# Kernel optimization log

Hardware: AMD Instinct MI355X
Metric: run time of the kernel (lower is better)

## Reference

```python
import jax, jax.numpy as jnp
import numpy as np

N, E, F, D, H, HID, OUT, G = 25000, 400000, 128, 16, 64, 128, 32, 64

def silu(v):
    return v * jax.nn.sigmoid(v)

def setup_inputs() -> dict:
    key = jax.random.key(0)
    ks = jax.random.split(key, 32)
    inp = {
        'x': jax.random.normal(ks[0], (N, F), jnp.float32),
        'pos': jax.random.normal(ks[1], (N, 3), jnp.float32),
        'edge_attr': jax.random.normal(ks[2], (E, D), jnp.float32),
        'edge_index': jax.random.randint(ks[3], (2, E), 0, N, jnp.int64),
        'batch': jnp.sort(jax.random.randint(ks[4], (N,), 0, G, jnp.int64)),
    }
    def lin(k, fan_in, fan_out):
        return jax.random.normal(k, (fan_in, fan_out), jnp.float32) / np.sqrt(fan_in)
    i = 5
    for l, in_c in enumerate([F, HID]):
        cat = 2 * in_c + D + 1
        inp[f'l{l}_mlp_w'] = lin(ks[i], cat, H); i += 1
        inp[f'l{l}_edge_w'] = lin(ks[i], H, H); i += 1
        inp[f'l{l}_edge_b'] = jnp.zeros((H,), jnp.float32)
        inp[f'l{l}_coord_w'] = lin(ks[i], H, 1); i += 1
        inp[f'l{l}_coord_b'] = jnp.zeros((1,), jnp.float32)
        inp[f'l{l}_node_w1'] = lin(ks[i], in_c + H, H); i += 1
        inp[f'l{l}_node_b1'] = jnp.zeros((H,), jnp.float32)
        inp[f'l{l}_node_w2'] = lin(ks[i], H, HID); i += 1
        inp[f'l{l}_node_b2'] = jnp.zeros((HID,), jnp.float32)
    inp['out_w1'] = lin(ks[i], HID, HID); i += 1
    inp['out_b1'] = jnp.zeros((HID,), jnp.float32)
    inp['out_w2'] = lin(ks[i], HID, OUT); i += 1
    inp['out_b2'] = jnp.zeros((OUT,), jnp.float32)
    return inp

def egnn_layer(x, pos, src, dst, edge_attr, mlp_w, edge_w, edge_b, coord_w, coord_b, nw1, nb1, nw2, nb2):
    # PyG flow source_to_target: i = dst (edge_index[1]), j = src (edge_index[0])
    diff = pos[dst] - pos[src]                    # (E,3)
    radial = jnp.sum(diff * diff, axis=1, keepdims=True)  # (E,1)
    cat = jnp.concatenate([x[dst], x[src], edge_attr, radial], axis=1)
    h = silu(cat @ mlp_w)                         # (E,H)
    e_ij = silu(h @ edge_w + edge_b)              # (E,H)
    coord_update = diff * silu(e_ij @ coord_w + coord_b)  # (E,3)
    e_agg = jax.ops.segment_sum(e_ij, dst, num_segments=N)          # sum reduce
    cu_sum = jax.ops.segment_sum(coord_update, dst, num_segments=N)
    deg = jax.ops.segment_sum(jnp.ones((E, 1), x.dtype), dst, num_segments=N)
    cu_mean = cu_sum / jnp.maximum(deg, 1.0)      # mean reduce, 0 for isolated nodes
    h_node = silu(jnp.concatenate([x, e_agg], axis=1) @ nw1 + nb1) @ nw2 + nb2
    return h_node, pos + cu_mean

def reference(x, pos, edge_attr, edge_index, batch,
              l0_mlp_w, l0_edge_w, l0_edge_b, l0_coord_w, l0_coord_b, l0_node_w1, l0_node_b1, l0_node_w2, l0_node_b2,
              l1_mlp_w, l1_edge_w, l1_edge_b, l1_coord_w, l1_coord_b, l1_node_w1, l1_node_b1, l1_node_w2, l1_node_b2,
              out_w1, out_b1, out_w2, out_b2):
    src, dst = edge_index[0], edge_index[1]
    x, pos = egnn_layer(x, pos, src, dst, edge_attr, l0_mlp_w, l0_edge_w, l0_edge_b, l0_coord_w, l0_coord_b, l0_node_w1, l0_node_b1, l0_node_w2, l0_node_b2)
    x, pos = egnn_layer(x, pos, src, dst, edge_attr, l1_mlp_w, l1_edge_w, l1_edge_b, l1_coord_w, l1_coord_b, l1_node_w1, l1_node_b1, l1_node_w2, l1_node_b2)
    # graph mean pooling over batch assignment
    g_sum = jax.ops.segment_sum(x, batch, num_segments=G)
    g_cnt = jax.ops.segment_sum(jnp.ones((N, 1), x.dtype), batch, num_segments=G)
    g = g_sum / jnp.maximum(g_cnt, 1.0)           # (G, HID)
    g = jax.nn.relu(g)
    return jax.nn.relu(g @ out_w1 + out_b1) @ out_w2 + out_b2  # (G, OUT)
```

## Files before the change

kernel.cpp:

```cpp
#include <hip/hip_runtime.h>
#include <math.h>

#define NN 25000
#define EE 400000
#define FF 128
#define DD 16
#define HH 64
#define HIDC 128
#define OUTC 32
#define GG 64
#define NODEBLK 782
#define SCATBLK 1563

typedef __attribute__((ext_vector_type(8))) short short8;
typedef __attribute__((ext_vector_type(8))) unsigned short u16x8;
typedef __attribute__((ext_vector_type(4))) float f32x4;

union S8 { short8 v; unsigned short u[8]; };
union U8 { u16x8 v; unsigned short u[8]; };

__device__ __forceinline__ float silu_f(float v) {
    return v / (1.f + __expf(-v));
}

__device__ __forceinline__ unsigned short f2bf_rne(float f) {
  unsigned u = __float_as_uint(f);
  unsigned r = u + 0x7fffu + ((u >> 16) & 1u);
  return (unsigned short)(r >> 16);
}
__device__ __forceinline__ float bfbits2f(unsigned short b) {
  return __uint_as_float(((unsigned)b) << 16);
}

__global__ __launch_bounds__(256) void k_hist(
    const int* __restrict__ ei, int* __restrict__ cnt) {
  const int t = blockIdx.x * 256 + threadIdx.x;
  if (t < EE) atomicAdd(&cnt[ei[EE + t]], 1);
}

__global__ __launch_bounds__(1024) void k_scan(
    const int* __restrict__ cnt, int* __restrict__ row_ptr, int* __restrict__ next) {
  __shared__ int s[1024];
  const int t = threadIdx.x;
  const int base = t * 25;
  int loc[25];
  int sum = 0;
#pragma unroll
  for (int i = 0; i < 25; ++i) {
    const int n = base + i;
    loc[i] = (n < NN) ? cnt[n] : 0;
    sum += loc[i];
  }
  s[t] = sum;
  __syncthreads();
  for (int off = 1; off < 1024; off <<= 1) {
    const int v = (t >= off) ? s[t - off] : 0;
    __syncthreads();
    s[t] += v;
    __syncthreads();
  }
  int run = s[t] - sum;
#pragma unroll
  for (int i = 0; i < 25; ++i) {
    const int n = base + i;
    if (n < NN) {
      row_ptr[n] = run;
      next[n] = run;
      run += loc[i];
    }
  }
  if (t == 0) row_ptr[NN] = EE;
}

__global__ __launch_bounds__(256) void k_sp(
    const int* __restrict__ ei, int* __restrict__ next,
    int* __restrict__ sdst, int* __restrict__ ssrc, int* __restrict__ seid,
    const float* __restrict__ X, const float* __restrict__ W,
    float* __restrict__ P1, unsigned short* __restrict__ P2h) {
  __shared__ __align__(16) float xT[4][128 * 12];
  if (blockIdx.x >= NODEBLK) {
    const int t = (blockIdx.x - NODEBLK) * 256 + threadIdx.x;
    if (t < EE) {
      const int d = ei[EE + t];
      const int slot = atomicAdd(&next[d], 1);
      sdst[slot] = d;
      ssrc[slot] = ei[t];
      seid[slot] = t;
    }
    return;
  }
  const int w = threadIdx.x >> 6, lane = threadIdx.x & 63;
  float* xt = xT[w];
  const int nb = (blockIdx.x * 4 + w) * 8;
#pragma unroll
  for (int e = 0; e < 8; ++e) {
    const int n = nb + e;
    const bool v = n < NN;
    xt[lane * 12 + e]        = v ? X[n * FF + lane] : 0.f;
    xt[(lane + 64) * 12 + e] = v ? X[n * FF + 64 + lane] : 0.f;
  }
  __syncthreads();
  float a1[8], a2[8];
#pragma unroll
  for (int e = 0; e < 8; ++e) { a1[e] = 0.f; a2[e] = 0.f; }
#pragma unroll 4
  for (int k = 0; k < 128; ++k) {
    const float wa = W[k * 64 + lane];
    const float wb = W[(128 + k) * 64 + lane];
    float xk[8];
    *(f32x4*)&xk[0] = *(const f32x4*)&xt[k * 12];
    *(f32x4*)&xk[4] = *(const f32x4*)&xt[k * 12 + 4];
#pragma unroll
    for (int e = 0; e < 8; ++e) {
      a1[e] = fmaf(xk[e], wa, a1[e]);
      a2[e] = fmaf(xk[e], wb, a2[e]);
    }
  }
#pragma unroll
  for (int e = 0; e < 8; ++e) {
    const int n = nb + e;
    if (n < NN) {
      P1[n * 64 + lane]  = a1[e];
      P2h[n * 64 + lane] = f2bf_rne(a2[e]);
    }
  }
}

template <bool COORD, bool GATHER>
__global__ __launch_bounds__(256, 4) void k_edge(
    const float* __restrict__ P1, const unsigned short* __restrict__ P2h,
    const float* __restrict__ pos, const float* __restrict__ eattr,
    float* __restrict__ seattr, const int* __restrict__ seid,
    const int* __restrict__ sdst, const int* __restrict__ ssrc,
    const float* __restrict__ mlp_w,
    const float* __restrict__ edge_w, const float* __restrict__ edge_b,
    const float* __restrict__ coord_w, const float* __restrict__ coord_b,
    float* __restrict__ e_agg, float* __restrict__ cu) {
  __shared__ __align__(16) float s_hs[4][16 * 76];
  __shared__ float s_diff[4][48];
  __shared__ float s_rad[4][16];
  __shared__ float s_red[4][16];
  const int tid = threadIdx.x, w = tid >> 6, lane = tid & 63;
  const int q = lane >> 4, m = lane & 15;

  S8 wB[2][4];
#pragma unroll
  for (int kc = 0; kc < 2; ++kc)
#pragma unroll
    for (int nc = 0; nc < 4; ++nc)
#pragma unroll
      for (int j = 0; j < 8; ++j)
        wB[kc][nc].u[j] = f2bf_rne(edge_w[(kc * 32 + q * 8 + j) * 64 + nc * 16 + m]);
  S8 w3B[4];
#pragma unroll
  for (int nc = 0; nc < 4; ++nc)
#pragma unroll
    for (int j = 0; j < 8; ++j)
      w3B[nc].u[j] = (lane < 32) ? f2bf_rne(mlp_w[256 * 64 + (q * 8 + j) * 64 + nc * 16 + m])
                                 : (unsigned short)0;
  float w4r[4], cwr[4], ebr[4];
#pragma unroll
  for (int nc = 0; nc < 4; ++nc) {
    w4r[nc] = mlp_w[272 * 64 + nc * 16 + m];
    ebr[nc] = edge_b[nc * 16 + m];
    cwr[nc] = COORD ? coord_w[nc * 16 + m] : 0.f;
  }
  const float cb = COORD ? coord_b[0] : 0.f;

  const int wave_id = blockIdx.x * 4 + w;
  const int g0 = wave_id * 6 + (wave_id < 424 ? wave_id : 424);
  const int ng = (wave_id < 424) ? 7 : 6;

  const int pe = (lane < 48) ? (lane / 3) : 0;
  const int pc = lane - (lane / 3) * 3;

  int cur_dst = -1;
  float accum = 0.f;

  for (int g = 0; g < ng; ++g) {
    const int eb = (g0 + g) * 16;
    const int dm = sdst[eb + m];
    const int sm = ssrc[eb + m];
    f32x4 p1a[2], p1b[2];
    U8 p2r[2];
#pragma unroll
    for (int kc = 0; kc < 2; ++kc) {
      const float* pp1 = P1 + (size_t)dm * 64 + kc * 32 + q * 8;
      p1a[kc] = *(const f32x4*)pp1;
      p1b[kc] = *(const f32x4*)(pp1 + 4);
      p2r[kc].v = *(const u16x8*)(P2h + (size_t)sm * 64 + kc * 32 + q * 8);
    }
    if (lane < 48) {
      const int de = __shfl(dm, pe, 64), se = __shfl(sm, pe, 64);
      s_diff[w][lane] = pos[de * 3 + pc] - pos[se * 3 + pc];
    }
    f32x4 ea0 = {0.f, 0.f, 0.f, 0.f}, ea1 = {0.f, 0.f, 0.f, 0.f};
    if (lane < 32) {
      if (GATHER) {
        const int eid = seid[eb + m];
        const float* ep = &eattr[(size_t)eid * DD + q * 8];
        ea0 = *(const f32x4*)ep;
        ea1 = *(const f32x4*)(ep + 4);
        float* sp = &seattr[(size_t)(eb + m) * DD + q * 8];
        *(f32x4*)sp = ea0;
        *(f32x4*)(sp + 4) = ea1;
      } else {
        const float* ep = &seattr[(size_t)(eb + m) * DD + q * 8];
        ea0 = *(const f32x4*)ep;
        ea1 = *(const f32x4*)(ep + 4);
      }
    }
    S8 eaA;
#pragma unroll
    for (int j = 0; j < 4; ++j) {
      eaA.u[j]     = f2bf_rne(ea0[j]);
      eaA.u[4 + j] = f2bf_rne(ea1[j]);
    }
    if (lane < 16) {
      const float d0 = s_diff[w][lane * 3 + 0];
      const float d1 = s_diff[w][lane * 3 + 1];
      const float d2 = s_diff[w][lane * 3 + 2];
      s_rad[w][lane] = fmaf(d0, d0, fmaf(d1, d1, d2 * d2));
    }
    float radr[4];
#pragma unroll
    for (int r = 0; r < 4; ++r) radr[r] = s_rad[w][q * 4 + r];
    f32x4 c3[4];
#pragma unroll
    for (int nc = 0; nc < 4; ++nc) {
      f32x4 z = {0.f, 0.f, 0.f, 0.f};
      c3[nc] = __builtin_amdgcn_mfma_f32_16x16x32_bf16(eaA.v, w3B[nc].v, z, 0, 0, 0);
    }
#pragma unroll
    for (int nc = 0; nc < 4; ++nc)
#pragma unroll
      for (int r = 0; r < 4; ++r)
        s_hs[w][(q * 4 + r) * 76 + nc * 16 + m] = fmaf(radr[r], w4r[nc], c3[nc][r]);
    S8 ahi[2], alo[2];
#pragma unroll
    for (int kc = 0; kc < 2; ++kc) {
      const float* hp = &s_hs[w][m * 76 + kc * 32 + q * 8];
      f32x4 h0 = *(const f32x4*)hp;
      f32x4 h1 = *(const f32x4*)(hp + 4);
      h0 = h0 + p1a[kc];
      h1 = h1 + p1b[kc];
      float hv[8];
      *(f32x4*)&hv[0] = h0;
      *(f32x4*)&hv[4] = h1;
#pragma unroll
      for (int j = 0; j < 8; ++j) {
        const float h = silu_f(hv[j] + bfbits2f(p2r[kc].u[j]));
        const unsigned short hb = (unsigned short)(__float_as_uint(h) >> 16);
        ahi[kc].u[j] = hb;
        alo[kc].u[j] = f2bf_rne(h - bfbits2f(hb));
      }
    }
    f32x4 o[4];
#pragma unroll
    for (int nc = 0; nc < 4; ++nc) {
      f32x4 bi = {ebr[nc], ebr[nc], ebr[nc], ebr[nc]};
      o[nc] = bi;
    }
#pragma unroll
    for (int kc = 0; kc < 2; ++kc)
#pragma unroll
      for (int nc = 0; nc < 4; ++nc) {
        o[nc] = __builtin_amdgcn_mfma_f32_16x16x32_bf16(ahi[kc].v, wB[kc][nc].v, o[nc], 0, 0, 0);
        o[nc] = __builtin_amdgcn_mfma_f32_16x16x32_bf16(alo[kc].v, wB[kc][nc].v, o[nc], 0, 0, 0);
      }
#pragma unroll
    for (int nc = 0; nc < 4; ++nc)
#pragma unroll
      for (int r = 0; r < 4; ++r) o[nc][r] = silu_f(o[nc][r]);
    if (COORD) {
#pragma unroll
      for (int r = 0; r < 4; ++r) {
        float v = o[0][r] * cwr[0] + o[1][r] * cwr[1] + o[2][r] * cwr[2] + o[3][r] * cwr[3];
        v += __shfl_xor(v, 1, 64);
        v += __shfl_xor(v, 2, 64);
        v += __shfl_xor(v, 4, 64);
        v += __shfl_xor(v, 8, 64);
        if (m == 0) s_red[w][q * 4 + r] = v;
      }
    }
#pragma unroll
    for (int nc = 0; nc < 4; ++nc)
#pragma unroll
      for (int r = 0; r < 4; ++r)
        s_hs[w][(q * 4 + r) * 76 + nc * 16 + m] = o[nc][r];
    for (int e = 0; e < 16; ++e) {
      const int dv = __shfl(dm, e, 64);
      const float v = s_hs[w][e * 76 + lane];
      if (dv == cur_dst) {
        accum += v;
      } else {
        if (cur_dst >= 0) atomicAdd(&e_agg[(size_t)cur_dst * 64 + lane], accum);
        cur_dst = dv;
        accum = v;
      }
    }
    if (COORD) {
      if (lane < 48) {
        const float s = silu_f(s_red[w][pe] + cb);
        atomicAdd(&cu[(size_t)__shfl(dm, pe, 64) * 3 + pc], s_diff[w][lane] * s);
      }
    }
  }
  if (cur_dst >= 0) atomicAdd(&e_agg[(size_t)cur_dst * 64 + lane], accum);
}

__global__ __launch_bounds__(256) void k_node_l0(
    const float* __restrict__ x_in, float* __restrict__ e_agg,
    const float* __restrict__ nw1, const float* __restrict__ nb1,
    const float* __restrict__ nw2, const float* __restrict__ nb2,
    const float* __restrict__ pos_in, const float* __restrict__ cu,
    const int* __restrict__ row_ptr,
    float* __restrict__ x_out, float* __restrict__ pos_out,
    const float* __restrict__ Wn, float* __restrict__ P1,
    unsigned short* __restrict__ P2h) {
  __shared__ __align__(16) float xT[4][192 * 12];
  const int w = threadIdx.x >> 6, lane = threadIdx.x & 63;
  float* xt = xT[w];
  const int nb = (blockIdx.x * 4 + w) * 8;
#pragma unroll
  for (int e = 0; e < 8; ++e) {
    const int n = nb + e;
    const bool v = n < NN;
    xt[lane * 12 + e]         = v ? x_in[n * HIDC + lane] : 0.f;
    xt[(64 + lane) * 12 + e]  = v ? x_in[n * HIDC + 64 + lane] : 0.f;
    xt[(128 + lane) * 12 + e] = v ? e_agg[n * 64 + lane] : 0.f;
    if (v) e_agg[n * 64 + lane] = 0.f;
  }
  __syncthreads();
  float a[8];
#pragma unroll
  for (int e = 0; e < 8; ++e) a[e] = nb1[lane];
#pragma unroll 2
  for (int k = 0; k < 192; ++k) {
    const float wv = nw1[k * 64 + lane];
    float xk[8];
    *(f32x4*)&xk[0] = *(const f32x4*)&xt[k * 12];
    *(f32x4*)&xk[4] = *(const f32x4*)&xt[k * 12 + 4];
#pragma unroll
    for (int e = 0; e < 8; ++e) a[e] = fmaf(xk[e], wv, a[e]);
  }
#pragma unroll
  for (int e = 0; e < 8; ++e) a[e] = silu_f(a[e]);
  {
    f32x4 t0 = {a[0], a[1], a[2], a[3]};
    f32x4 t1 = {a[4], a[5], a[6], a[7]};
    *(f32x4*)&xt[lane * 12]     = t0;
    *(f32x4*)&xt[lane * 12 + 4] = t1;
  }
  float olo[8], ohi[8];
#pragma unroll
  for (int e = 0; e < 8; ++e) { olo[e] = nb2[lane]; ohi[e] = nb2[64 + lane]; }
#pragma unroll 2
  for (int k = 0; k < 64; ++k) {
    const float wl = nw2[k * HIDC + lane];
    const float wh = nw2[k * HIDC + 64 + lane];
    float hk[8];
    *(f32x4*)&hk[0] = *(const f32x4*)&xt[k * 12];
    *(f32x4*)&hk[4] = *(const f32x4*)&xt[k * 12 + 4];
#pragma unroll
    for (int e = 0; e < 8; ++e) {
      olo[e] = fmaf(hk[e], wl, olo[e]);
      ohi[e] = fmaf(hk[e], wh, ohi[e]);
    }
  }
#pragma unroll
  for (int e = 0; e < 8; ++e) {
    const int n = nb + e;
    if (n < NN) {
      x_out[n * HIDC + lane]      = olo[e];
      x_out[n * HIDC + 64 + lane] = ohi[e];
    }
  }
#pragma unroll
  for (int e = 0; e < 8; ++e) {
    const int n = nb + e;
    if (n < NN && lane < 3) {
      const float dg = fmaxf((float)(row_ptr[n + 1] - row_ptr[n]), 1.f);
      pos_out[n * 3 + lane] = pos_in[n * 3 + lane] + cu[n * 3 + lane] / dg;
    }
  }
  {
    f32x4 t0 = {olo[0], olo[1], olo[2], olo[3]};
    f32x4 t1 = {olo[4], olo[5], olo[6], olo[7]};
    *(f32x4*)&xt[lane * 12]     = t0;
    *(f32x4*)&xt[lane * 12 + 4] = t1;
    f32x4 t2 = {ohi[0], ohi[1], ohi[2], ohi[3]};
    f32x4 t3 = {ohi[4], ohi[5], ohi[6], ohi[7]};
    *(f32x4*)&xt[(64 + lane) * 12]     = t2;
    *(f32x4*)&xt[(64 + lane) * 12 + 4] = t3;
  }
  float a1[8], a2[8];
#pragma unroll
  for (int e = 0; e < 8; ++e) { a1[e] = 0.f; a2[e] = 0.f; }
#pragma unroll 4
  for (int k = 0; k < 128; ++k) {
    const float wa = Wn[k * 64 + lane];
    const float wb2 = Wn[(128 + k) * 64 + lane];
    float xk[8];
    *(f32x4*)&xk[0] = *(const f32x4*)&xt[k * 12];
    *(f32x4*)&xk[4] = *(const f32x4*)&xt[k * 12 + 4];
#pragma unroll
    for (int e = 0; e < 8; ++e) {
      a1[e] = fmaf(xk[e], wa, a1[e]);
      a2[e] = fmaf(xk[e], wb2, a2[e]);
    }
  }
#pragma unroll
  for (int e = 0; e < 8; ++e) {
    const int n = nb + e;
    if (n < NN) {
      P1[n * 64 + lane]  = a1[e];
      P2h[n * 64 + lane] = f2bf_rne(a2[e]);
    }
  }
}

__global__ __launch_bounds__(256) void k_node_l1(
    const float* __restrict__ x_in, const float* __restrict__ e_agg,
    const float* __restrict__ nw1, const float* __restrict__ nb1,
    const float* __restrict__ nw2, const float* __restrict__ nb2,
    const int* __restrict__ batch,
    float* __restrict__ g_sum, float* __restrict__ g_cnt) {
  __shared__ __align__(16) float xT[4][192 * 12];
  const int w = threadIdx.x >> 6, lane = threadIdx.x & 63;
  float* xt = xT[w];
  const int nb = (blockIdx.x * 4 + w) * 8;
#pragma unroll
  for (int e = 0; e < 8; ++e) {
    const int n = nb + e;
    const bool v = n < NN;
    xt[lane * 12 + e]         = v ? x_in[n * HIDC + lane] : 0.f;
    xt[(64 + lane) * 12 + e]  = v ? x_in[n * HIDC + 64 + lane] : 0.f;
    xt[(128 + lane) * 12 + e] = v ? e_agg[n * 64 + lane] : 0.f;
  }
  __syncthreads();
  float a[8];
#pragma unroll
  for (int e = 0; e < 8; ++e) a[e] = nb1[lane];
#pragma unroll 2
  for (int k = 0; k < 192; ++k) {
    const float wv = nw1[k * 64 + lane];
    float xk[8];
    *(f32x4*)&xk[0] = *(const f32x4*)&xt[k * 12];
    *(f32x4*)&xk[4] = *(const f32x4*)&xt[k * 12 + 4];
#pragma unroll
    for (int e = 0; e < 8; ++e) a[e] = fmaf(xk[e], wv, a[e]);
  }
#pragma unroll
  for (int e = 0; e < 8; ++e) a[e] = silu_f(a[e]);
  {
    f32x4 t0 = {a[0], a[1], a[2], a[3]};
    f32x4 t1 = {a[4], a[5], a[6], a[7]};
    *(f32x4*)&xt[lane * 12]     = t0;
    *(f32x4*)&xt[lane * 12 + 4] = t1;
  }
  float olo[8], ohi[8];
#pragma unroll
  for (int e = 0; e < 8; ++e) { olo[e] = nb2[lane]; ohi[e] = nb2[64 + lane]; }
#pragma unroll 2
  for (int k = 0; k < 64; ++k) {
    const float wl = nw2[k * HIDC + lane];
    const float wh = nw2[k * HIDC + 64 + lane];
    float hk[8];
    *(f32x4*)&hk[0] = *(const f32x4*)&xt[k * 12];
    *(f32x4*)&hk[4] = *(const f32x4*)&xt[k * 12 + 4];
#pragma unroll
    for (int e = 0; e < 8; ++e) {
      olo[e] = fmaf(hk[e], wl, olo[e]);
      ohi[e] = fmaf(hk[e], wh, ohi[e]);
    }
  }
  int curb = -1;
  float accL = 0.f, accH = 0.f, c = 0.f;
#pragma unroll
  for (int e = 0; e < 8; ++e) {
    const int n = nb + e;
    if (n < NN) {
      const int bg = batch[n];
      if (bg != curb) {
        if (curb >= 0) {
          atomicAdd(&g_sum[curb * HIDC + lane], accL);
          atomicAdd(&g_sum[curb * HIDC + 64 + lane], accH);
          if (lane == 0) atomicAdd(&g_cnt[curb], c);
        }
        curb = bg; accL = olo[e]; accH = ohi[e]; c = 1.f;
      } else {
        accL += olo[e]; accH += ohi[e]; c += 1.f;
      }
    }
  }
  if (curb >= 0) {
    atomicAdd(&g_sum[curb * HIDC + lane], accL);
    atomicAdd(&g_sum[curb * HIDC + 64 + lane], accH);
    if (lane == 0) atomicAdd(&g_cnt[curb], c);
  }
}

__global__ __launch_bounds__(128) void k_final(
    const float* __restrict__ g_sum, const float* __restrict__ g_cnt,
    const float* __restrict__ w1, const float* __restrict__ b1,
    const float* __restrict__ w2, const float* __restrict__ b2,
    float* __restrict__ out) {
  __shared__ float sg[128];
  __shared__ float sh[128];
  const int g = blockIdx.x, j = threadIdx.x;
  const float c = fmaxf(g_cnt[g], 1.f);
  sg[j] = fmaxf(g_sum[g * HIDC + j] / c, 0.f);
  __syncthreads();
  float a = b1[j];
  for (int k = 0; k < 128; ++k) a += sg[k] * w1[k * 128 + j];
  sh[j] = fmaxf(a, 0.f);
  __syncthreads();
  if (j < OUTC) {
    float o = b2[j];
    for (int k = 0; k < 128; ++k) o += sh[k] * w2[k * OUTC + j];
    out[g * OUTC + j] = o;
  }
}

extern "C" void kernel_launch(void* const* d_in, const int* in_sizes, int n_in,
                              void* d_out, int out_size, void* d_ws, size_t ws_size,
                              hipStream_t stream) {
  const float* x     = (const float*)d_in[0];
  const float* pos   = (const float*)d_in[1];
  const float* eattr = (const float*)d_in[2];
  const int*   ei    = (const int*)d_in[3];
  const int*   batch = (const int*)d_in[4];
  const float* mlp_w[2]   = {(const float*)d_in[5],  (const float*)d_in[14]};
  const float* edge_w[2]  = {(const float*)d_in[6],  (const float*)d_in[15]};
  const float* edge_b[2]  = {(const float*)d_in[7],  (const float*)d_in[16]};
  const float* coord_w[2] = {(const float*)d_in[8],  (const float*)d_in[17]};
  const float* coord_b[2] = {(const float*)d_in[9],  (const float*)d_in[18]};
  const float* nw1[2]     = {(const float*)d_in[10], (const float*)d_in[19]};
  const float* nb1[2]     = {(const float*)d_in[11], (const float*)d_in[20]};
  const float* nw2[2]     = {(const float*)d_in[12], (const float*)d_in[21]};
  const float* nb2[2]     = {(const float*)d_in[13], (const float*)d_in[22]};
  const float* ow1 = (const float*)d_in[23];
  const float* ob1 = (const float*)d_in[24];
  const float* ow2 = (const float*)d_in[25];
  const float* ob2 = (const float*)d_in[26];
  float* out = (float*)d_out;

  char* p = (char*)d_ws;
  auto alloc = [&](size_t bytes) {
    void* r = (void*)p;
    p += (bytes + 255) & ~(size_t)255;
    return r;
  };
  float* P1            = (float*)alloc((size_t)NN * 64 * 4);
  unsigned short* P2h  = (unsigned short*)alloc((size_t)NN * 64 * 2);
  char* zero_base      = p;
  float* e_agg         = (float*)alloc((size_t)NN * 64 * 4);
  float* cu            = (float*)alloc((size_t)NN * 3 * 4);
  float* g_sum         = (float*)alloc((size_t)GG * HIDC * 4);
  float* g_cnt         = (float*)alloc((size_t)GG * 4);
  int* cnt             = (int*)alloc((size_t)NN * 4);
  const size_t zero_sz = (size_t)(p - zero_base);
  int* row_ptr         = (int*)alloc((size_t)(NN + 1) * 4);
  int* nxt             = (int*)alloc((size_t)NN * 4);
  int* sdst            = (int*)alloc((size_t)EE * 4);
  int* ssrc            = (int*)alloc((size_t)EE * 4);
  int* seid            = (int*)alloc((size_t)EE * 4);
  float* seattr        = (float*)alloc((size_t)EE * DD * 4);
  float* x1            = (float*)alloc((size_t)NN * HIDC * 4);
  float* pos1          = (float*)alloc((size_t)NN * 3 * 4);

  const int edgeBlocks = 1024;

  (void)hipMemsetAsync(zero_base, 0, zero_sz, stream);

  k_hist<<<SCATBLK, 256, 0, stream>>>(ei, cnt);
  k_scan<<<1, 1024, 0, stream>>>(cnt, row_ptr, nxt);
  k_sp<<<NODEBLK + SCATBLK, 256, 0, stream>>>(ei, nxt, sdst, ssrc, seid,
      x, mlp_w[0], P1, P2h);

  k_edge<true, true><<<edgeBlocks, 256, 0, stream>>>(P1, P2h, pos, eattr,
      seattr, seid, sdst, ssrc, mlp_w[0], edge_w[0], edge_b[0],
      coord_w[0], coord_b[0], e_agg, cu);
  k_node_l0<<<NODEBLK, 256, 0, stream>>>(x, e_agg, nw1[0], nb1[0],
      nw2[0], nb2[0], pos, cu, row_ptr, x1, pos1, mlp_w[1], P1, P2h);

  k_edge<false, false><<<edgeBlocks, 256, 0, stream>>>(P1, P2h, pos1, eattr,
      seattr, seid, sdst, ssrc, mlp_w[1], edge_w[1], edge_b[1],
      coord_w[1], coord_b[1], e_agg, cu);
  k_node_l1<<<NODEBLK, 256, 0, stream>>>(x1, e_agg, nw1[1], nb1[1],
      nw2[1], nb2[1], batch, g_sum, g_cnt);

  k_final<<<GG, 128, 0, stream>>>(g_sum, g_cnt, ow1, ob1, ow2, ob2, out);
}
```

Baseline: 507.9 us.

## Move node MLPs to split-bf16 MFMA and store edge attributes as bf16

```diff
diff --git a/kernel.cpp b/kernel.cpp
--- a/kernel.cpp
+++ b/kernel.cpp
@@ -11,6 +11,7 @@
 #define GG 64
 #define NODEBLK 782
 #define SCATBLK 1563
+#define NTILES 1563
 
 typedef __attribute__((ext_vector_type(8))) short short8;
 typedef __attribute__((ext_vector_type(8))) unsigned short u16x8;
@@ -30,6 +31,35 @@
 }
 __device__ __forceinline__ float bfbits2f(unsigned short b) {
   return __uint_as_float(((unsigned)b) << 16);
+}
+
+__device__ __forceinline__ void split8(const float* hv, S8& hi, S8& lo) {
+#pragma unroll
+  for (int j = 0; j < 8; ++j) {
+    const unsigned short hb = (unsigned short)(__float_as_uint(hv[j]) >> 16);
+    hi.u[j] = hb;
+    lo.u[j] = f2bf_rne(hv[j] - bfbits2f(hb));
+  }
+}
+
+__device__ __forceinline__ void loadBsplit(const float* __restrict__ W, int ldw,
+                                           int k0, int n0, int q, int m,
+                                           S8& bh, S8& bl) {
+#pragma unroll
+  for (int j = 0; j < 8; ++j) {
+    const float wv = W[(size_t)(k0 + q * 8 + j) * ldw + n0 + m];
+    const unsigned short hb = (unsigned short)(__float_as_uint(wv) >> 16);
+    bh.u[j] = hb;
+    bl.u[j] = f2bf_rne(wv - bfbits2f(hb));
+  }
+}
+
+__device__ __forceinline__ f32x4 mfma3(const S8& ah, const S8& al,
+                                       const S8& bh, const S8& bl, f32x4 c) {
+  c = __builtin_amdgcn_mfma_f32_16x16x32_bf16(ah.v, bh.v, c, 0, 0, 0);
+  c = __builtin_amdgcn_mfma_f32_16x16x32_bf16(al.v, bh.v, c, 0, 0, 0);
+  c = __builtin_amdgcn_mfma_f32_16x16x32_bf16(ah.v, bl.v, c, 0, 0, 0);
+  return c;
 }
 
 __global__ __launch_bounds__(256) void k_hist(
@@ -130,7 +160,7 @@
 __global__ __launch_bounds__(256, 4) void k_edge(
     const float* __restrict__ P1, const unsigned short* __restrict__ P2h,
     const float* __restrict__ pos, const float* __restrict__ eattr,
-    float* __restrict__ seattr, const int* __restrict__ seid,
+    unsigned short* __restrict__ seattr_h, const int* __restrict__ seid,
     const int* __restrict__ sdst, const int* __restrict__ ssrc,
     const float* __restrict__ mlp_w,
     const float* __restrict__ edge_w, const float* __restrict__ edge_b,
@@ -194,27 +224,24 @@
       const int de = __shfl(dm, pe, 64), se = __shfl(sm, pe, 64);
       s_diff[w][lane] = pos[de * 3 + pc] - pos[se * 3 + pc];
     }
-    f32x4 ea0 = {0.f, 0.f, 0.f, 0.f}, ea1 = {0.f, 0.f, 0.f, 0.f};
+    S8 eaA;
+#pragma unroll
+    for (int j = 0; j < 8; ++j) eaA.u[j] = 0;
     if (lane < 32) {
       if (GATHER) {
         const int eid = seid[eb + m];
         const float* ep = &eattr[(size_t)eid * DD + q * 8];
-        ea0 = *(const f32x4*)ep;
-        ea1 = *(const f32x4*)(ep + 4);
-        float* sp = &seattr[(size_t)(eb + m) * DD + q * 8];
-        *(f32x4*)sp = ea0;
-        *(f32x4*)(sp + 4) = ea1;
+        const f32x4 ea0 = *(const f32x4*)ep;
+        const f32x4 ea1 = *(const f32x4*)(ep + 4);
+#pragma unroll
+        for (int j = 0; j < 4; ++j) {
+          eaA.u[j]     = f2bf_rne(ea0[j]);
+          eaA.u[4 + j] = f2bf_rne(ea1[j]);
+        }
+        *(short8*)&seattr_h[(size_t)(eb + m) * DD + q * 8] = eaA.v;
       } else {
-        const float* ep = &seattr[(size_t)(eb + m) * DD + q * 8];
-        ea0 = *(const f32x4*)ep;
-        ea1 = *(const f32x4*)(ep + 4);
-      }
-    }
-    S8 eaA;
-#pragma unroll
-    for (int j = 0; j < 4; ++j) {
-      eaA.u[j]     = f2bf_rne(ea0[j]);
-      eaA.u[4 + j] = f2bf_rne(ea1[j]);
+        eaA.v = *(const short8*)&seattr_h[(size_t)(eb + m) * DD + q * 8];
+      }
     }
     if (lane < 16) {
       const float d0 = s_diff[w][lane * 3 + 0];
@@ -309,7 +336,8 @@
   if (cur_dst >= 0) atomicAdd(&e_agg[(size_t)cur_dst * 64 + lane], accum);
 }
 
-__global__ __launch_bounds__(256) void k_node_l0(
+template <bool L0>
+__global__ __launch_bounds__(256) void k_node(
     const float* __restrict__ x_in, float* __restrict__ e_agg,
     const float* __restrict__ nw1, const float* __restrict__ nb1,
     const float* __restrict__ nw2, const float* __restrict__ nb2,
@@ -317,187 +345,152 @@
     const int* __restrict__ row_ptr,
     float* __restrict__ x_out, float* __restrict__ pos_out,
     const float* __restrict__ Wn, float* __restrict__ P1,
-    unsigned short* __restrict__ P2h) {
-  __shared__ __align__(16) float xT[4][192 * 12];
-  const int w = threadIdx.x >> 6, lane = threadIdx.x & 63;
-  float* xt = xT[w];
-  const int nb = (blockIdx.x * 4 + w) * 8;
-#pragma unroll
-  for (int e = 0; e < 8; ++e) {
-    const int n = nb + e;
-    const bool v = n < NN;
-    xt[lane * 12 + e]         = v ? x_in[n * HIDC + lane] : 0.f;
-    xt[(64 + lane) * 12 + e]  = v ? x_in[n * HIDC + 64 + lane] : 0.f;
-    xt[(128 + lane) * 12 + e] = v ? e_agg[n * 64 + lane] : 0.f;
-    if (v) e_agg[n * 64 + lane] = 0.f;
-  }
-  __syncthreads();
-  float a[8];
-#pragma unroll
-  for (int e = 0; e < 8; ++e) a[e] = nb1[lane];
-#pragma unroll 2
-  for (int k = 0; k < 192; ++k) {
-    const float wv = nw1[k * 64 + lane];
-    float xk[8];
-    *(f32x4*)&xk[0] = *(const f32x4*)&xt[k * 12];
-    *(f32x4*)&xk[4] = *(const f32x4*)&xt[k * 12 + 4];
-#pragma unroll
-    for (int e = 0; e < 8; ++e) a[e] = fmaf(xk[e], wv, a[e]);
-  }
-#pragma unroll
-  for (int e = 0; e < 8; ++e) a[e] = silu_f(a[e]);
-  {
-    f32x4 t0 = {a[0], a[1], a[2], a[3]};
-    f32x4 t1 = {a[4], a[5], a[6], a[7]};
-    *(f32x4*)&xt[lane * 12]     = t0;
-    *(f32x4*)&xt[lane * 12 + 4] = t1;
-  }
-  float olo[8], ohi[8];
-#pragma unroll
-  for (int e = 0; e < 8; ++e) { olo[e] = nb2[lane]; ohi[e] = nb2[64 + lane]; }
-#pragma unroll 2
-  for (int k = 0; k < 64; ++k) {
-    const float wl = nw2[k * HIDC + lane];
-    const float wh = nw2[k * HIDC + 64 + lane];
-    float hk[8];
-    *(f32x4*)&hk[0] = *(const f32x4*)&xt[k * 12];
-    *(f32x4*)&hk[4] = *(const f32x4*)&xt[k * 12 + 4];
-#pragma unroll
-    for (int e = 0; e < 8; ++e) {
-      olo[e] = fmaf(hk[e], wl, olo[e]);
-      ohi[e] = fmaf(hk[e], wh, ohi[e]);
-    }
-  }
-#pragma unroll
-  for (int e = 0; e < 8; ++e) {
-    const int n = nb + e;
-    if (n < NN) {
-      x_out[n * HIDC + lane]      = olo[e];
-      x_out[n * HIDC + 64 + lane] = ohi[e];
-    }
-  }
-#pragma unroll
-  for (int e = 0; e < 8; ++e) {
-    const int n = nb + e;
-    if (n < NN && lane < 3) {
-      const float dg = fmaxf((float)(row_ptr[n + 1] - row_ptr[n]), 1.f);
-      pos_out[n * 3 + lane] = pos_in[n * 3 + lane] + cu[n * 3 + lane] / dg;
-    }
-  }
-  {
-    f32x4 t0 = {olo[0], olo[1], olo[2], olo[3]};
-    f32x4 t1 = {olo[4], olo[5], olo[6], olo[7]};
-    *(f32x4*)&xt[lane * 12]     = t0;
-    *(f32x4*)&xt[lane * 12 + 4] = t1;
-    f32x4 t2 = {ohi[0], ohi[1], ohi[2], ohi[3]};
-    f32x4 t3 = {ohi[4], ohi[5], ohi[6], ohi[7]};
-    *(f32x4*)&xt[(64 + lane) * 12]     = t2;
-    *(f32x4*)&xt[(64 + lane) * 12 + 4] = t3;
-  }
-  float a1[8], a2[8];
-#pragma unroll
-  for (int e = 0; e < 8; ++e) { a1[e] = 0.f; a2[e] = 0.f; }
-#pragma unroll 4
-  for (int k = 0; k < 128; ++k) {
-    const float wa = Wn[k * 64 + lane];
-    const float wb2 = Wn[(128 + k) * 64 + lane];
-    float xk[8];
-    *(f32x4*)&xk[0] = *(const f32x4*)&xt[k * 12];
-    *(f32x4*)&xk[4] = *(const f32x4*)&xt[k * 12 + 4];
-#pragma unroll
-    for (int e = 0; e < 8; ++e) {
-      a1[e] = fmaf(xk[e], wa, a1[e]);
-      a2[e] = fmaf(xk[e], wb2, a2[e]);
-    }
-  }
-#pragma unroll
-  for (int e = 0; e < 8; ++e) {
-    const int n = nb + e;
-    if (n < NN) {
-      P1[n * 64 + lane]  = a1[e];
-      P2h[n * 64 + lane] = f2bf_rne(a2[e]);
-    }
-  }
-}
-
-__global__ __launch_bounds__(256) void k_node_l1(
-    const float* __restrict__ x_in, const float* __restrict__ e_agg,
-    const float* __restrict__ nw1, const float* __restrict__ nb1,
-    const float* __restrict__ nw2, const float* __restrict__ nb2,
+    unsigned short* __restrict__ P2h,
     const int* __restrict__ batch,
     float* __restrict__ g_sum, float* __restrict__ g_cnt) {
-  __shared__ __align__(16) float xT[4][192 * 12];
-  const int w = threadIdx.x >> 6, lane = threadIdx.x & 63;
-  float* xt = xT[w];
-  const int nb = (blockIdx.x * 4 + w) * 8;
-#pragma unroll
-  for (int e = 0; e < 8; ++e) {
-    const int n = nb + e;
-    const bool v = n < NN;
-    xt[lane * 12 + e]         = v ? x_in[n * HIDC + lane] : 0.f;
-    xt[(64 + lane) * 12 + e]  = v ? x_in[n * HIDC + 64 + lane] : 0.f;
-    xt[(128 + lane) * 12 + e] = v ? e_agg[n * 64 + lane] : 0.f;
-  }
-  __syncthreads();
-  float a[8];
-#pragma unroll
-  for (int e = 0; e < 8; ++e) a[e] = nb1[lane];
-#pragma unroll 2
-  for (int k = 0; k < 192; ++k) {
-    const float wv = nw1[k * 64 + lane];
-    float xk[8];
-    *(f32x4*)&xk[0] = *(const f32x4*)&xt[k * 12];
-    *(f32x4*)&xk[4] = *(const f32x4*)&xt[k * 12 + 4];
-#pragma unroll
-    for (int e = 0; e < 8; ++e) a[e] = fmaf(xk[e], wv, a[e]);
-  }
-#pragma unroll
-  for (int e = 0; e < 8; ++e) a[e] = silu_f(a[e]);
-  {
-    f32x4 t0 = {a[0], a[1], a[2], a[3]};
-    f32x4 t1 = {a[4], a[5], a[6], a[7]};
-    *(f32x4*)&xt[lane * 12]     = t0;
-    *(f32x4*)&xt[lane * 12 + 4] = t1;
-  }
-  float olo[8], ohi[8];
-#pragma unroll
-  for (int e = 0; e < 8; ++e) { olo[e] = nb2[lane]; ohi[e] = nb2[64 + lane]; }
-#pragma unroll 2
-  for (int k = 0; k < 64; ++k) {
-    const float wl = nw2[k * HIDC + lane];
-    const float wh = nw2[k * HIDC + 64 + lane];
-    float hk[8];
-    *(f32x4*)&hk[0] = *(const f32x4*)&xt[k * 12];
-    *(f32x4*)&hk[4] = *(const f32x4*)&xt[k * 12 + 4];
-#pragma unroll
-    for (int e = 0; e < 8; ++e) {
-      olo[e] = fmaf(hk[e], wl, olo[e]);
-      ohi[e] = fmaf(hk[e], wh, ohi[e]);
-    }
-  }
-  int curb = -1;
-  float accL = 0.f, accH = 0.f, c = 0.f;
-#pragma unroll
-  for (int e = 0; e < 8; ++e) {
-    const int n = nb + e;
-    if (n < NN) {
-      const int bg = batch[n];
-      if (bg != curb) {
-        if (curb >= 0) {
-          atomicAdd(&g_sum[curb * HIDC + lane], accL);
-          atomicAdd(&g_sum[curb * HIDC + 64 + lane], accH);
-          if (lane == 0) atomicAdd(&g_cnt[curb], c);
+  __shared__ __align__(16) float sbuf[4][16 * 132];
+  const int tid = threadIdx.x, w = tid >> 6, lane = tid & 63;
+  const int q = lane >> 4, m = lane & 15;
+  const int tile = blockIdx.x * 4 + w;
+  if (tile >= NTILES) return;
+  const int n0 = tile * 16;
+  const int nm = n0 + m;
+  const bool vm = nm < NN;
+  float* sb = sbuf[w];
+
+  S8 axh[6], axl[6];
+#pragma unroll
+  for (int kc = 0; kc < 6; ++kc) {
+    float hv[8] = {0.f, 0.f, 0.f, 0.f, 0.f, 0.f, 0.f, 0.f};
+    if (vm) {
+      const float* src = (kc < 4) ? (x_in + (size_t)nm * HIDC + kc * 32 + q * 8)
+                                  : (e_agg + (size_t)nm * 64 + (kc - 4) * 32 + q * 8);
+      *(f32x4*)&hv[0] = *(const f32x4*)src;
+      *(f32x4*)&hv[4] = *(const f32x4*)(src + 4);
+    }
+    split8(hv, axh[kc], axl[kc]);
+  }
+  if (L0 && vm) {
+    const f32x4 z = {0.f, 0.f, 0.f, 0.f};
+    float* ez = e_agg + (size_t)nm * 64 + q * 8;
+    *(f32x4*)ez = z; *(f32x4*)(ez + 4) = z;
+    *(f32x4*)(ez + 32) = z; *(f32x4*)(ez + 36) = z;
+  }
+#pragma unroll
+  for (int nc = 0; nc < 4; ++nc) {
+    const float b = nb1[nc * 16 + m];
+    f32x4 acc = {b, b, b, b};
+#pragma unroll
+    for (int kc = 0; kc < 6; ++kc) {
+      S8 bh, bl;
+      loadBsplit(nw1, 64, kc * 32, nc * 16, q, m, bh, bl);
+      acc = mfma3(axh[kc], axl[kc], bh, bl, acc);
+    }
+#pragma unroll
+    for (int r = 0; r < 4; ++r)
+      sb[(q * 4 + r) * 132 + nc * 16 + m] = silu_f(acc[r]);
+  }
+  S8 ah[2], al[2];
+#pragma unroll
+  for (int kc = 0; kc < 2; ++kc) {
+    float hv[8];
+    const float* hp = &sb[m * 132 + kc * 32 + q * 8];
+    *(f32x4*)&hv[0] = *(const f32x4*)hp;
+    *(f32x4*)&hv[4] = *(const f32x4*)(hp + 4);
+    split8(hv, ah[kc], al[kc]);
+  }
+  f32x4 hh[8];
+#pragma unroll
+  for (int nc = 0; nc < 8; ++nc) {
+    const float b = nb2[nc * 16 + m];
+    f32x4 acc = {b, b, b, b};
+#pragma unroll
+    for (int kc = 0; kc < 2; ++kc) {
+      S8 bh, bl;
+      loadBsplit(nw2, 128, kc * 32, nc * 16, q, m, bh, bl);
+      acc = mfma3(ah[kc], al[kc], bh, bl, acc);
+    }
+    hh[nc] = acc;
+  }
+  if (L0) {
+#pragma unroll
+    for (int nc = 0; nc < 8; ++nc)
+#pragma unroll
+      for (int r = 0; r < 4; ++r) {
+        const int n = n0 + q * 4 + r;
+        sb[(q * 4 + r) * 132 + nc * 16 + m] = hh[nc][r];
+        if (n < NN) x_out[(size_t)n * HIDC + nc * 16 + m] = hh[nc][r];
+      }
+    if (lane < 48) {
+      const int pe2 = lane / 3, pc2 = lane - pe2 * 3;
+      const int n = n0 + pe2;
+      if (n < NN) {
+        const float dg = fmaxf((float)(row_ptr[n + 1] - row_ptr[n]), 1.f);
+        pos_out[n * 3 + pc2] = pos_in[n * 3 + pc2] + cu[n * 3 + pc2] / dg;
+      }
+    }
+    S8 a1h[4], a1l[4];
+#pragma unroll
+    for (int kc = 0; kc < 4; ++kc) {
+      float hv[8];
+      const float* hp = &sb[m * 132 + kc * 32 + q * 8];
+      *(f32x4*)&hv[0] = *(const f32x4*)hp;
+      *(f32x4*)&hv[4] = *(const f32x4*)(hp + 4);
+      split8(hv, a1h[kc], a1l[kc]);
+    }
+#pragma unroll
+    for (int nc = 0; nc < 8; ++nc) {
+      const float* Wb = Wn + (size_t)(nc < 4 ? 0 : 128 * 64);
+      const int ncc = nc & 3;
+      f32x4 acc = {0.f, 0.f, 0.f, 0.f};
+#pragma unroll
+      for (int kc = 0; kc < 4; ++kc) {
+        S8 bh, bl;
+        loadBsplit(Wb, 64, kc * 32, ncc * 16, q, m, bh, bl);
+        acc = mfma3(a1h[kc], a1l[kc], bh, bl, acc);
+      }
+#pragma unroll
+      for (int r = 0; r < 4; ++r) {
+        const int n = n0 + q * 4 + r;
+        if (n < NN) {
+          if (nc < 4) P1[(size_t)n * 64 + ncc * 16 + m] = acc[r];
+          else        P2h[(size_t)n * 64 + ncc * 16 + m] = f2bf_rne(acc[r]);
         }
-        curb = bg; accL = olo[e]; accH = ohi[e]; c = 1.f;
-      } else {
-        accL += olo[e]; accH += ohi[e]; c += 1.f;
-      }
-    }
-  }
-  if (curb >= 0) {
-    atomicAdd(&g_sum[curb * HIDC + lane], accL);
-    atomicAdd(&g_sum[curb * HIDC + 64 + lane], accH);
-    if (lane == 0) atomicAdd(&g_cnt[curb], c);
+      }
+    }
+  } else {
+    int curb = -1;
+    float cnt2 = 0.f;
+    float pacc[8];
+#pragma unroll
+    for (int r = 0; r < 4; ++r) {
+      const int n = n0 + q * 4 + r;
+      if (n < NN) {
+        const int bg = batch[n];
+        if (bg != curb) {
+          if (curb >= 0) {
+#pragma unroll
+            for (int nc = 0; nc < 8; ++nc)
+              atomicAdd(&g_sum[curb * HIDC + nc * 16 + m], pacc[nc]);
+            if (m == 0) atomicAdd(&g_cnt[curb], cnt2);
+          }
+          curb = bg;
+#pragma unroll
+          for (int nc = 0; nc < 8; ++nc) pacc[nc] = hh[nc][r];
+          cnt2 = 1.f;
+        } else {
+#pragma unroll
+          for (int nc = 0; nc < 8; ++nc) pacc[nc] += hh[nc][r];
+          cnt2 += 1.f;
+        }
+      }
+    }
+    if (curb >= 0) {
+#pragma unroll
+      for (int nc = 0; nc < 8; ++nc)
+        atomicAdd(&g_sum[curb * HIDC + nc * 16 + m], pacc[nc]);
+      if (m == 0) atomicAdd(&g_cnt[curb], cnt2);
+    }
   }
 }
 
@@ -566,11 +559,12 @@
   int* sdst            = (int*)alloc((size_t)EE * 4);
   int* ssrc            = (int*)alloc((size_t)EE * 4);
   int* seid            = (int*)alloc((size_t)EE * 4);
-  float* seattr        = (float*)alloc((size_t)EE * DD * 4);
+  unsigned short* seah = (unsigned short*)alloc((size_t)EE * DD * 2);
   float* x1            = (float*)alloc((size_t)NN * HIDC * 4);
   float* pos1          = (float*)alloc((size_t)NN * 3 * 4);
 
   const int edgeBlocks = 1024;
+  const int nodeTileBlk = (NTILES + 3) / 4;
 
   (void)hipMemsetAsync(zero_base, 0, zero_sz, stream);
 
@@ -580,16 +574,18 @@
       x, mlp_w[0], P1, P2h);
 
   k_edge<true, true><<<edgeBlocks, 256, 0, stream>>>(P1, P2h, pos, eattr,
-      seattr, seid, sdst, ssrc, mlp_w[0], edge_w[0], edge_b[0],
+      seah, seid, sdst, ssrc, mlp_w[0], edge_w[0], edge_b[0],
       coord_w[0], coord_b[0], e_agg, cu);
-  k_node_l0<<<NODEBLK, 256, 0, stream>>>(x, e_agg, nw1[0], nb1[0],
-      nw2[0], nb2[0], pos, cu, row_ptr, x1, pos1, mlp_w[1], P1, P2h);
+  k_node<true><<<nodeTileBlk, 256, 0, stream>>>(x, e_agg, nw1[0], nb1[0],
+      nw2[0], nb2[0], pos, cu, row_ptr, x1, pos1, mlp_w[1], P1, P2h,
+      batch, g_sum, g_cnt);
 
   k_edge<false, false><<<edgeBlocks, 256, 0, stream>>>(P1, P2h, pos1, eattr,
-      seattr, seid, sdst, ssrc, mlp_w[1], edge_w[1], edge_b[1],
+      seah, seid, sdst, ssrc, mlp_w[1], edge_w[1], edge_b[1],
       coord_w[1], coord_b[1], e_agg, cu);
-  k_node_l1<<<NODEBLK, 256, 0, stream>>>(x1, e_agg, nw1[1], nb1[1],
-      nw2[1], nb2[1], batch, g_sum, g_cnt);
+  k_node<false><<<nodeTileBlk, 256, 0, stream>>>(x1, e_agg, nw1[1], nb1[1],
+      nw2[1], nb2[1], pos1, cu, row_ptr, x1, pos1, mlp_w[1], P1, P2h,
+      batch, g_sum, g_cnt);
 
   k_final<<<GG, 128, 0, stream>>>(g_sum, g_cnt, ow1, ob1, ow2, ob2, out);
 }
```

New measurement: 471.8 us. 1.08x faster.
